# Performance work log

Hardware: AMD Instinct MI355X
Metric: run time of the kernel (lower is better)

The kernel has to match this reference:

```python
import jax, jax.numpy as jnp
import numpy as np

LOG_CLAMP = -100.0  # torch.nn.BCELoss clamps log terms at -100


def setup_inputs() -> dict:
    key = jax.random.key(0)
    k1, k2 = jax.random.split(key)
    shape = (64, 8, 65536, 1)  # [B, C, H, W]
    vertical_pred = jax.random.uniform(k1, shape, dtype=jnp.float32)
    vertical_true = jax.random.uniform(k2, shape, dtype=jnp.float32)
    return {"vertical_pred": vertical_pred, "vertical_true": vertical_true}


def reference(vertical_pred, vertical_true):
    # Only the first width column is used: [B, C, H]
    p = vertical_pred[..., 0]
    t = vertical_true[..., 0]
    log_p = jnp.clip(jnp.log(p), LOG_CLAMP)
    log_1mp = jnp.clip(jnp.log1p(-p), LOG_CLAMP)
    bce = -(t * log_p + (1.0 - t) * log_1mp)           # [B, C, H]
    per_bc = jnp.mean(bce, axis=-1)                     # mean over H per (b, c)
    loss = jnp.sum(per_bc) / vertical_pred.shape[0]     # sum over b,c then / B
    return loss
```

## Files before the change

kernel.cpp:

```cpp
#include <hip/hip_runtime.h>


#define LOG2_CLAMP -144.26950408889634f

__device__ __forceinline__ void bce4_acc(const float4& p, const float4& t,
                                         float& sq, float& sd) {
    float lp, lq;
    lp = fmaxf(__log2f(p.x), LOG2_CLAMP);
    lq = fmaxf(__log2f(1.0f - p.x), LOG2_CLAMP);
    sq += lq; sd = __builtin_fmaf(t.x, lp - lq, sd);
    lp = fmaxf(__log2f(p.y), LOG2_CLAMP);
    lq = fmaxf(__log2f(1.0f - p.y), LOG2_CLAMP);
    sq += lq; sd = __builtin_fmaf(t.y, lp - lq, sd);
    lp = fmaxf(__log2f(p.z), LOG2_CLAMP);
    lq = fmaxf(__log2f(1.0f - p.z), LOG2_CLAMP);
    sq += lq; sd = __builtin_fmaf(t.z, lp - lq, sd);
    lp = fmaxf(__log2f(p.w), LOG2_CLAMP);
    lq = fmaxf(__log2f(1.0f - p.w), LOG2_CLAMP);
    sq += lq; sd = __builtin_fmaf(t.w, lp - lq, sd);
}

__global__ __launch_bounds__(256) void vertical_loss_kernel(
    const float4* __restrict__ p4,
    const float4* __restrict__ t4,
    float* __restrict__ out,
    int n4, float final_scale)
{
    float sq = 0.0f, sd = 0.0f;

    const int chunk = n4 / (int)gridDim.x;
    const int steps = chunk / (int)blockDim.x;

    if ((chunk % (int)blockDim.x) == 0 && (steps & 3) == 0 && steps >= 8) {
        const int stp = (int)blockDim.x;
        int i = (int)blockIdx.x * chunk + (int)threadIdx.x;

        float4 P0 = p4[i], P1 = p4[i + stp], P2 = p4[i + 2 * stp], P3 = p4[i + 3 * stp];
        float4 T0 = t4[i], T1 = t4[i + stp], T2 = t4[i + 2 * stp], T3 = t4[i + 3 * stp];

        const int groups = steps >> 2;
        for (int g = 1; g < groups; ++g) {
            i += 4 * stp;
            __builtin_amdgcn_sched_barrier(0);
            float4 Q0 = p4[i], Q1 = p4[i + stp], Q2 = p4[i + 2 * stp], Q3 = p4[i + 3 * stp];
            float4 U0 = t4[i], U1 = t4[i + stp], U2 = t4[i + 2 * stp], U3 = t4[i + 3 * stp];
            __builtin_amdgcn_sched_barrier(0);
            bce4_acc(P0, T0, sq, sd);
            bce4_acc(P1, T1, sq, sd);
            bce4_acc(P2, T2, sq, sd);
            bce4_acc(P3, T3, sq, sd);
            P0 = Q0; P1 = Q1; P2 = Q2; P3 = Q3;
            T0 = U0; T1 = U1; T2 = U2; T3 = U3;
        }
        bce4_acc(P0, T0, sq, sd);
        bce4_acc(P1, T1, sq, sd);
        bce4_acc(P2, T2, sq, sd);
        bce4_acc(P3, T3, sq, sd);
    } else {
        for (int i = (int)blockIdx.x * (int)blockDim.x + (int)threadIdx.x;
             i < n4; i += (int)gridDim.x * (int)blockDim.x)
            bce4_acc(p4[i], t4[i], sq, sd);
    }

    float sum = sq + sd;

    #pragma unroll
    for (int off = 32; off > 0; off >>= 1)
        sum += __shfl_down(sum, off, 64);

    __shared__ float wsum[4];
    int wave = threadIdx.x >> 6;
    int lane = threadIdx.x & 63;
    if (lane == 0) wsum[wave] = sum;
    __syncthreads();

    if (threadIdx.x == 0) {
        float s = wsum[0] + wsum[1] + wsum[2] + wsum[3];
        atomicAdd(out, s * final_scale);
    }
}

extern "C" void kernel_launch(void* const* d_in, const int* in_sizes, int n_in,
                              void* d_out, int out_size, void* d_ws, size_t ws_size,
                              hipStream_t stream) {
    const float4* pred  = (const float4*)d_in[0];
    const float4* true_ = (const float4*)d_in[1];
    float* out = (float*)d_out;

    int n  = in_sizes[0];
    int n4 = n / 4;
    float final_scale = -0.69314718055994531f / (65536.0f * 64.0f);

    hipMemsetAsync(d_out, 0, sizeof(float), stream);

    int blocks = 2048;
    vertical_loss_kernel<<<blocks, 256, 0, stream>>>(pred, true_, out, n4, final_scale);
}
```

Baseline: 278.4 us.

## Stream inputs through double-buffered LDS via async global-to-LDS loads

Replaces the register-prefetched float4 loop with a pipeline that copies 2048-float tiles of both inputs straight into LDS using global_load_lds, double-buffered so the next tile loads while the current one is reduced. The grid shrinks to 1024 blocks of 128 threads, and a scalar tail path is added for sizes that are not multiples of four. The goal is to keep loads outstanding without register pressure. The cost is extra block-level barriers, LDS occupancy limits, and fewer threads in flight.

Measured after the change: 279.8 us. No clear change (+0.5%).

```diff
diff --git a/kernel.cpp b/kernel.cpp
--- a/kernel.cpp
+++ b/kernel.cpp
@@ -2,8 +2,13 @@
 
 
 #define LOG2_CLAMP -144.26950408889634f
+#define TILE 2048
+#define THREADS 128
 
-__device__ __forceinline__ void bce4_acc(const float4& p, const float4& t,
+typedef __attribute__((address_space(1))) void GV;
+typedef __attribute__((address_space(3))) void LV;
+
+__device__ __forceinline__ void bce4_acc(float4 p, float4 t,
                                          float& sq, float& sd) {
     float lp, lq;
     lp = fmaxf(__log2f(p.x), LOG2_CLAMP);
@@ -20,79 +25,100 @@
     sq += lq; sd = __builtin_fmaf(t.w, lp - lq, sd);
 }
 
-__global__ __launch_bounds__(256) void vertical_loss_kernel(
-    const float4* __restrict__ p4,
-    const float4* __restrict__ t4,
+__global__ __launch_bounds__(THREADS) void vertical_loss_kernel(
+    const float* __restrict__ pf,
+    const float* __restrict__ tf,
     float* __restrict__ out,
-    int n4, float final_scale)
+    int n, float final_scale)
 {
+    __shared__ float Pb[2][TILE];
+    __shared__ float Tb[2][TILE];
+
+    const int tid  = threadIdx.x;
+    const int wave = tid >> 6;
+    const int lane = tid & 63;
+
     float sq = 0.0f, sd = 0.0f;
 
-    const int chunk = n4 / (int)gridDim.x;
-    const int steps = chunk / (int)blockDim.x;
+    const long long total = (long long)n;
+    const int perBlockFloats = (int)(total / (long long)gridDim.x);
+    const int iters = perBlockFloats / TILE;
 
-    if ((chunk % (int)blockDim.x) == 0 && (steps & 3) == 0 && steps >= 8) {
-        const int stp = (int)blockDim.x;
-        int i = (int)blockIdx.x * chunk + (int)threadIdx.x;
+    if ((total % ((long long)gridDim.x * TILE)) == 0 && iters > 0) {
+        const long long blockBase = (long long)blockIdx.x * perBlockFloats;
 
-        float4 P0 = p4[i], P1 = p4[i + stp], P2 = p4[i + 2 * stp], P3 = p4[i + 3 * stp];
-        float4 T0 = t4[i], T1 = t4[i + stp], T2 = t4[i + 2 * stp], T3 = t4[i + 3 * stp];
+        auto stage = [&](int b, int it) {
+            const float* gp = pf + blockBase + (long long)it * TILE;
+            const float* gt = tf + blockBase + (long long)it * TILE;
+            #pragma unroll
+            for (int j = 0; j < 4; ++j) {
+                const int s = wave * 4 + j;
+                const int o = s * 256 + lane * 4;
+                __builtin_amdgcn_global_load_lds((GV*)(gp + o),
+                                                 (LV*)(&Pb[b][s * 256]),
+                                                 16, 0, 0);
+                __builtin_amdgcn_global_load_lds((GV*)(gt + o),
+                                                 (LV*)(&Tb[b][s * 256]),
+                                                 16, 0, 0);
+            }
+        };
 
-        const int groups = steps >> 2;
-        for (int g = 1; g < groups; ++g) {
-            i += 4 * stp;
-            __builtin_amdgcn_sched_barrier(0);
-            float4 Q0 = p4[i], Q1 = p4[i + stp], Q2 = p4[i + 2 * stp], Q3 = p4[i + 3 * stp];
-            float4 U0 = t4[i], U1 = t4[i + stp], U2 = t4[i + 2 * stp], U3 = t4[i + 3 * stp];
-            __builtin_amdgcn_sched_barrier(0);
-            bce4_acc(P0, T0, sq, sd);
-            bce4_acc(P1, T1, sq, sd);
-            bce4_acc(P2, T2, sq, sd);
-            bce4_acc(P3, T3, sq, sd);
-            P0 = Q0; P1 = Q1; P2 = Q2; P3 = Q3;
-            T0 = U0; T1 = U1; T2 = U2; T3 = U3;
+        stage(0, 0);
+        for (int it = 0; it < iters; ++it) {
+            const int b = it & 1;
+            if (it + 1 < iters) stage(b ^ 1, it + 1);
+            __syncthreads();
+            const float4* P4 = (const float4*)Pb[b];
+            const float4* T4 = (const float4*)Tb[b];
+            #pragma unroll
+            for (int k = 0; k < 4; ++k) {
+                float4 p = P4[k * THREADS + tid];
+                float4 t = T4[k * THREADS + tid];
+                bce4_acc(p, t, sq, sd);
+            }
+            __syncthreads();
         }
-        bce4_acc(P0, T0, sq, sd);
-        bce4_acc(P1, T1, sq, sd);
-        bce4_acc(P2, T2, sq, sd);
-        bce4_acc(P3, T3, sq, sd);
     } else {
-        for (int i = (int)blockIdx.x * (int)blockDim.x + (int)threadIdx.x;
-             i < n4; i += (int)gridDim.x * (int)blockDim.x)
+        const float4* p4 = (const float4*)pf;
+        const float4* t4 = (const float4*)tf;
+        const int n4 = n >> 2;
+        for (int i = (int)blockIdx.x * THREADS + tid; i < n4;
+             i += (int)gridDim.x * THREADS)
             bce4_acc(p4[i], t4[i], sq, sd);
+        if (blockIdx.x == 0 && tid == 0) {
+            for (int i = n4 << 2; i < n; ++i) {
+                float p = pf[i], t = tf[i];
+                float lp = fmaxf(__log2f(p), LOG2_CLAMP);
+                float lq = fmaxf(__log2f(1.0f - p), LOG2_CLAMP);
+                sq += lq; sd = __builtin_fmaf(t, lp - lq, sd);
+            }
+        }
     }
 
     float sum = sq + sd;
-
     #pragma unroll
     for (int off = 32; off > 0; off >>= 1)
         sum += __shfl_down(sum, off, 64);
 
-    __shared__ float wsum[4];
-    int wave = threadIdx.x >> 6;
-    int lane = threadIdx.x & 63;
-    if (lane == 0) wsum[wave] = sum;
     __syncthreads();
-
-    if (threadIdx.x == 0) {
-        float s = wsum[0] + wsum[1] + wsum[2] + wsum[3];
-        atomicAdd(out, s * final_scale);
-    }
+    if (lane == 0) Pb[0][wave] = sum;
+    __syncthreads();
+    if (tid == 0)
+        atomicAdd(out, (Pb[0][0] + Pb[0][1]) * final_scale);
 }
 
 extern "C" void kernel_launch(void* const* d_in, const int* in_sizes, int n_in,
                               void* d_out, int out_size, void* d_ws, size_t ws_size,
                               hipStream_t stream) {
-    const float4* pred  = (const float4*)d_in[0];
-    const float4* true_ = (const float4*)d_in[1];
+    const float* pred  = (const float*)d_in[0];
+    const float* true_ = (const float*)d_in[1];
     float* out = (float*)d_out;
 
-    int n  = in_sizes[0];
-    int n4 = n / 4;
+    int n = in_sizes[0];
     float final_scale = -0.69314718055994531f / (65536.0f * 64.0f);
 
     hipMemsetAsync(d_out, 0, sizeof(float), stream);
 
-    int blocks = 2048;
-    vertical_loss_kernel<<<blocks, 256, 0, stream>>>(pred, true_, out, n4, final_scale);
+    int blocks = 1024;
+    vertical_loss_kernel<<<blocks, THREADS, 0, stream>>>(pred, true_, out, n, final_scale);
 }
```
